# Kernel optimization log

Measured on AMD Instinct MI355X. Metric: run time of the kernel, lower is better.

The kernel has to match this reference:

```python
import jax, jax.numpy as jnp
import numpy as np

EPS = 1e-6

def _ln(x):
    # LayerNorm without affine, biased variance (matches torch default)
    m = jnp.mean(x, axis=-1, keepdims=True)
    v = jnp.var(x, axis=-1, keepdims=True)
    return (x - m) / jnp.sqrt(v + EPS)

def setup_inputs() -> dict:
    key = jax.random.key(0)
    ks = jax.random.split(key, 12)
    B, N, C = 8, 4096, 768
    H = C * 4
    s = 0.02
    return {
        "x":   jax.random.normal(ks[0], (B, N, C), dtype=jnp.float32),
        "Wq":  jax.random.normal(ks[1], (C, C), dtype=jnp.float32) * s,
        "bq":  jnp.zeros((C,), dtype=jnp.float32),
        "Wkv": jax.random.normal(ks[2], (C, 2 * C), dtype=jnp.float32) * s,
        "bkv": jnp.zeros((2 * C,), dtype=jnp.float32),
        "Wo":  jax.random.normal(ks[3], (C, C), dtype=jnp.float32) * s,
        "bo":  jnp.zeros((C,), dtype=jnp.float32),
        "W1":  jax.random.normal(ks[4], (C, H), dtype=jnp.float32) * s,
        "b1":  jnp.zeros((H,), dtype=jnp.float32),
        "W2":  jax.random.normal(ks[5], (H, C), dtype=jnp.float32) * s,
        "b2":  jnp.zeros((C,), dtype=jnp.float32),
    }

def reference(x, Wq, bq, Wkv, bkv, Wo, bo, W1, b1, W2, b2):
    B, N, C = x.shape
    h = 16
    d = C // h
    scale = d ** -0.5

    xn = _ln(x)                          # norm1 over full sequence
    past = xn[:, :-1, :]                 # [B, N-1, C]
    cur = xn[:, -1, :]                   # [B, C]

    q = (cur @ Wq + bq).reshape(B, h, 1, d)                 # [B,h,1,d]
    kv = past @ Wkv + bkv                                   # [B,N-1,2C]
    k, v = jnp.split(kv, 2, axis=-1)
    k = k.reshape(B, N - 1, h, d).transpose(0, 2, 1, 3)     # [B,h,N-1,d]
    v = v.reshape(B, N - 1, h, d).transpose(0, 2, 1, 3)

    sim = jnp.einsum('bhqd,bhkd->bhqk', q, k) * scale       # [B,h,1,N-1]
    attn = jax.nn.softmax(sim, axis=-1)
    out = jnp.einsum('bhqk,bhkd->bhqd', attn, v)            # [B,h,1,d]
    out = out.transpose(0, 2, 1, 3).reshape(B, C)           # [B,C]
    out = out @ Wo + bo

    last = x[:, -1, :] + out                                # attn residual
    mlp = jax.nn.gelu(_ln(last) @ W1 + b1, approximate=True) @ W2 + b2
    last = last + mlp                                       # mlp residual

    return x.at[:, -1, :].set(last)
```

## Files before the change

kernel.cpp:

```cpp
#include <hip/hip_runtime.h>

#define B_ 8
#define N_ 4096
#define C_ 768
#define NP_ 4095
#define H_ 16
#define D_ 48
#define HID_ 3072
#define SCALE 0.14433756729740643f

typedef unsigned short u16;
typedef unsigned int u32;
typedef __attribute__((ext_vector_type(4))) float f32x4;
typedef __attribute__((ext_vector_type(8))) short short8;

__device__ __forceinline__ u32 f2bf_bits(float f){
  union { float f; u32 i; } v; v.f = f;
  return (v.i + 0x7fffu + ((v.i >> 16) & 1u)) >> 16;
}
__device__ __forceinline__ u16 f2bf(float f){ return (u16)f2bf_bits(f); }
__device__ __forceinline__ u32 pack2(float a, float b){
  return f2bf_bits(a) | (f2bf_bits(b) << 16);
}

__global__ __launch_bounds__(256) void k_q(const float* __restrict__ x,
    const float* __restrict__ Wq, const float* __restrict__ bq,
    float* __restrict__ qv)
{
  int b = blockIdx.y, t = threadIdx.x;
  int j0 = blockIdx.x*32;
  __shared__ float xs[C_];
  __shared__ float red[32][9];
  __shared__ float redA[4], redB[4];
  const float* xr = x + ((size_t)b*N_ + NP_)*C_;
  float v0 = xr[t], v1 = xr[t+256], v2 = xr[t+512];
  float s = v0+v1+v2, q = v0*v0+v1*v1+v2*v2;
  #pragma unroll
  for (int off=32; off; off>>=1){ s += __shfl_xor(s,off); q += __shfl_xor(q,off); }
  int w = t>>6, l = t&63;
  if (l==0){ redA[w]=s; redB[w]=q; }
  __syncthreads();
  s = redA[0]+redA[1]+redA[2]+redA[3];
  q = redB[0]+redB[1]+redB[2]+redB[3];
  float mean = s*(1.f/C_), var = q*(1.f/C_) - mean*mean;
  float rstd = rsqrtf(var + 1e-6f);
  xs[t] = (v0-mean)*rstd; xs[t+256] = (v1-mean)*rstd; xs[t+512] = (v2-mean)*rstd;
  __syncthreads();
  int jl = t&31, part = t>>5;
  const float* wp = Wq + (size_t)(part*96)*C_ + j0 + jl;
  const float* xp = xs + part*96;
  float acc = 0.f;
  #pragma unroll 8
  for (int c=0;c<96;c++) acc += xp[c]*wp[(size_t)c*C_];
  red[jl][part] = acc;
  __syncthreads();
  if (part==0){
    float a = bq[j0+jl];
    #pragma unroll
    for (int p=0;p<8;p++) a += red[jl][p];
    qv[(size_t)b*C_ + j0 + jl] = a;
  }
}

__global__ __launch_bounds__(256) void k_qw(const float* __restrict__ qv,
    const float* __restrict__ Wkv, u16* __restrict__ qWb)
{
  int b = blockIdx.y, t = threadIdx.x;
  int c0 = blockIdx.x*16;
  __shared__ float qs[C_];
  for (int u=t; u<C_; u+=256) qs[u] = qv[(size_t)b*C_+u];
  __syncthreads();
  int h = t&15, cl = t>>4;
  int c = c0 + cl;
  const float* wp = Wkv + (size_t)c*(2*C_) + h*D_;
  const float* qh = qs + h*D_;
  float acc = 0.f;
  #pragma unroll
  for (int d=0; d<D_; d++) acc += qh[d]*wp[d];
  qWb[((size_t)b*H_ + h)*C_ + c] = f2bf(acc);
}

__global__ __launch_bounds__(256) void k_attn(const float* __restrict__ x,
    const u16* __restrict__ qWb, float* __restrict__ outp,
    float* __restrict__ ctx, float* __restrict__ denom)
{
  int b = blockIdx.y;
  int tid = threadIdx.x;
  int w = tid>>6, l = tid&63;
  int kblk = blockIdx.x*64;
  __shared__ float wexp[64][20];
  __shared__ float2 stl[64];
  const size_t xb = (size_t)b*N_*C_;

  #pragma unroll 4
  for (int it=0; it<16; ++it){
    int r = it*4 + w;
    int kt = kblk + r;
    const float4* rp = (const float4*)(x + xb + (size_t)kt*C_);
    float4* op = (float4*)(outp + xb + (size_t)kt*C_);
    float4 v0 = rp[l], v1 = rp[l+64], v2 = rp[l+128];
    op[l] = v0; op[l+64] = v1; op[l+128] = v2;
    float s = v0.x+v0.y+v0.z+v0.w + v1.x+v1.y+v1.z+v1.w + v2.x+v2.y+v2.z+v2.w;
    float q = v0.x*v0.x+v0.y*v0.y+v0.z*v0.z+v0.w*v0.w
            + v1.x*v1.x+v1.y*v1.y+v1.z*v1.z+v1.w*v1.w
            + v2.x*v2.x+v2.y*v2.y+v2.z*v2.z+v2.w*v2.w;
    #pragma unroll
    for (int off=32; off; off>>=1){ s += __shfl_xor(s,off); q += __shfl_xor(q,off); }
    if (l==0){
      float mean = s*(1.f/C_), var = q*(1.f/C_) - mean*mean;
      stl[r] = make_float2(mean, rsqrtf(var + 1e-6f));
    }
  }
  __syncthreads();

  {
    int arow = w*16 + (l&15);
    float2 ms = stl[arow];
    const float* ar = x + xb + (size_t)(kblk + arow)*C_ + (l>>4)*8;
    const u16* br = qWb + ((size_t)b*H_ + (l&15))*C_ + (l>>4)*8;
    f32x4 acc = {0.f,0.f,0.f,0.f};
    #pragma unroll 6
    for (int s2=0;s2<24;s2++){
      float4 g0 = *(const float4*)(ar + s2*32);
      float4 g1 = *(const float4*)(ar + s2*32 + 4);
      uint4 nv;
      nv.x = pack2((g0.x-ms.x)*ms.y, (g0.y-ms.x)*ms.y);
      nv.y = pack2((g0.z-ms.x)*ms.y, (g0.w-ms.x)*ms.y);
      nv.z = pack2((g1.x-ms.x)*ms.y, (g1.y-ms.x)*ms.y);
      nv.w = pack2((g1.z-ms.x)*ms.y, (g1.w-ms.x)*ms.y);
      union{uint4 u; short8 v;} A, Bf;
      A.u = nv;
      Bf.u = *(const uint4*)(br + s2*32);
      acc = __builtin_amdgcn_mfma_f32_16x16x32_bf16(A.v, Bf.v, acc, 0,0,0);
    }
    int hh = l&15, mb = (l>>4)*4;
    #pragma unroll
    for (int r=0;r<4;r++){
      int rr = w*16 + mb + r;
      int kt = kblk + rr;
      wexp[rr][hh] = (kt < NP_) ? __expf(acc[r]*SCALE) : 0.f;
    }
  }
  __syncthreads();

  if (tid < 16){
    float ds = 0.f;
    #pragma unroll 8
    for (int k=0;k<64;k++) ds += wexp[k][tid];
    atomicAdd(denom + (size_t)b*H_ + tid, ds);
  }

  int c0 = w*192;
  float accA[H_], accB[H_], accC[H_];
  #pragma unroll
  for (int h=0;h<H_;h++){ accA[h]=0.f; accB[h]=0.f; accC[h]=0.f; }
  for (int k=0;k<64;k++){
    int kt = kblk + k;
    const float* xr = x + xb + (size_t)kt*C_ + c0;
    float2 ms = stl[k];
    float xA = (xr[l]     - ms.x)*ms.y;
    float xB = (xr[l+64]  - ms.x)*ms.y;
    float xC = (xr[l+128] - ms.x)*ms.y;
    const float4* wp4 = (const float4*)&wexp[k][0];
    float4 w0 = wp4[0], w1 = wp4[1], w2 = wp4[2], w3 = wp4[3];
    accA[0]+=w0.x*xA; accA[1]+=w0.y*xA; accA[2]+=w0.z*xA; accA[3]+=w0.w*xA;
    accA[4]+=w1.x*xA; accA[5]+=w1.y*xA; accA[6]+=w1.z*xA; accA[7]+=w1.w*xA;
    accA[8]+=w2.x*xA; accA[9]+=w2.y*xA; accA[10]+=w2.z*xA; accA[11]+=w2.w*xA;
    accA[12]+=w3.x*xA; accA[13]+=w3.y*xA; accA[14]+=w3.z*xA; accA[15]+=w3.w*xA;
    accB[0]+=w0.x*xB; accB[1]+=w0.y*xB; accB[2]+=w0.z*xB; accB[3]+=w0.w*xB;
    accB[4]+=w1.x*xB; accB[5]+=w1.y*xB; accB[6]+=w1.z*xB; accB[7]+=w1.w*xB;
    accB[8]+=w2.x*xB; accB[9]+=w2.y*xB; accB[10]+=w2.z*xB; accB[11]+=w2.w*xB;
    accB[12]+=w3.x*xB; accB[13]+=w3.y*xB; accB[14]+=w3.z*xB; accB[15]+=w3.w*xB;
    accC[0]+=w0.x*xC; accC[1]+=w0.y*xC; accC[2]+=w0.z*xC; accC[3]+=w0.w*xC;
    accC[4]+=w1.x*xC; accC[5]+=w1.y*xC; accC[6]+=w1.z*xC; accC[7]+=w1.w*xC;
    accC[8]+=w2.x*xC; accC[9]+=w2.y*xC; accC[10]+=w2.z*xC; accC[11]+=w2.w*xC;
    accC[12]+=w3.x*xC; accC[13]+=w3.y*xC; accC[14]+=w3.z*xC; accC[15]+=w3.w*xC;
  }
  float* cb = ctx + (size_t)b*H_*C_;
  #pragma unroll
  for (int h=0;h<H_;h++){
    atomicAdd(cb + h*C_ + c0 + l,       accA[h]);
    atomicAdd(cb + h*C_ + c0 + 64 + l,  accB[h]);
    atomicAdd(cb + h*C_ + c0 + 128 + l, accC[h]);
  }
}

__global__ __launch_bounds__(256) void k_v(const float* __restrict__ ctx,
    const float* __restrict__ denom, const float* __restrict__ Wkv,
    const float* __restrict__ bkv, float* __restrict__ oat)
{
  int b = blockIdx.y, t = threadIdx.x;
  int t0 = blockIdx.x*32;
  int h0 = t0/D_;
  int h1 = (t0+31)/D_; if (h1 > H_-1) h1 = H_-1;
  __shared__ float cn[2][C_];
  __shared__ float red[32][9];
  float inv0 = 1.f/denom[(size_t)b*H_+h0];
  float inv1 = 1.f/denom[(size_t)b*H_+h1];
  for (int u=t; u<C_; u+=256){
    cn[0][u] = ctx[((size_t)b*H_+h0)*C_+u]*inv0;
    cn[1][u] = ctx[((size_t)b*H_+h1)*C_+u]*inv1;
  }
  __syncthreads();
  int jl = t&31, part = t>>5;
  int tt = t0 + jl;
  int hi = (tt/D_) - h0;
  const float* wp = Wkv + (size_t)(part*96)*(2*C_) + C_ + tt;
  const float* cp = cn[hi] + part*96;
  float acc = 0.f;
  #pragma unroll 8
  for (int c=0;c<96;c++) acc += cp[c]*wp[(size_t)c*(2*C_)];
  red[jl][part] = acc;
  __syncthreads();
  if (part==0){
    float a = bkv[C_ + tt];
    #pragma unroll
    for (int p=0;p<8;p++) a += red[jl][p];
    oat[(size_t)b*C_ + tt] = a;
  }
}

__global__ __launch_bounds__(256) void k_o(const float* __restrict__ x,
    const float* __restrict__ oat, const float* __restrict__ Wo,
    const float* __restrict__ bo, float* __restrict__ lastb)
{
  int b = blockIdx.y, t = threadIdx.x;
  int t0 = blockIdx.x*32;
  __shared__ float xs[C_];
  __shared__ float red[32][9];
  for (int u=t; u<C_; u+=256) xs[u] = oat[(size_t)b*C_+u];
  __syncthreads();
  int jl = t&31, part = t>>5;
  int tt = t0 + jl;
  const float* wp = Wo + (size_t)(part*96)*C_ + tt;
  const float* xp = xs + part*96;
  float acc = 0.f;
  #pragma unroll 8
  for (int c=0;c<96;c++) acc += xp[c]*wp[(size_t)c*C_];
  red[jl][part] = acc;
  __syncthreads();
  if (part==0){
    float a = bo[tt];
    #pragma unroll
    for (int p=0;p<8;p++) a += red[jl][p];
    lastb[(size_t)b*C_ + tt] = x[((size_t)b*N_ + NP_)*C_ + tt] + a;
  }
}

__global__ __launch_bounds__(256) void k_mlp1(const float* __restrict__ lastb,
    const float* __restrict__ W1, const float* __restrict__ b1,
    float* __restrict__ hid)
{
  int t = threadIdx.x;
  int j0 = blockIdx.x*16;
  __shared__ float xs[B_][C_];
  __shared__ float red[16][16][8];
  {
    int bb = t>>5, sub = t&31;
    const float* xr = lastb + (size_t)bb*C_;
    float s=0.f, q=0.f;
    #pragma unroll
    for (int j=0;j<24;j++){ float v = xr[sub+32*j]; s += v; q += v*v; }
    #pragma unroll
    for (int off=1; off<32; off<<=1){ s += __shfl_xor(s,off); q += __shfl_xor(q,off); }
    float mean = s*(1.f/C_), var = q*(1.f/C_) - mean*mean;
    float rstd = rsqrtf(var + 1e-6f);
    #pragma unroll
    for (int j=0;j<24;j++){ xs[bb][sub+32*j] = (xr[sub+32*j]-mean)*rstd; }
  }
  __syncthreads();
  int jl = t&15, part = t>>4;
  const float* wp = W1 + (size_t)(part*48)*HID_ + j0 + jl;
  float acc[B_];
  #pragma unroll
  for (int bb=0;bb<B_;bb++) acc[bb]=0.f;
  for (int c=0;c<48;c++){
    float wv = wp[(size_t)c*HID_];
    int cc = part*48 + c;
    #pragma unroll
    for (int bb=0;bb<B_;bb++) acc[bb] += xs[bb][cc]*wv;
  }
  #pragma unroll
  for (int bb=0;bb<B_;bb++) red[jl][part][bb] = acc[bb];
  __syncthreads();
  if (t < 128){
    int jl2 = t&15, bb = t>>4;
    float a = b1[j0+jl2];
    #pragma unroll
    for (int p=0;p<16;p++) a += red[jl2][p][bb];
    float t3 = a + 0.044715f*a*a*a;
    float g = 0.5f*a*(1.f + tanhf(0.7978845608f*t3));
    hid[(size_t)bb*HID_ + j0 + jl2] = g;
  }
}

__global__ __launch_bounds__(256) void k_mlp2(const float* __restrict__ hid,
    const float* __restrict__ W2, const float* __restrict__ b2,
    const float* __restrict__ lastb, float* __restrict__ outp)
{
  int t = threadIdx.x;
  int c0 = blockIdx.x*8;
  __shared__ float red[8][32][8];
  int ccl = t&7, part = t>>3;
  const float* wp = W2 + (size_t)(part*96)*C_ + c0 + ccl;
  float acc[B_];
  #pragma unroll
  for (int bb=0;bb<B_;bb++) acc[bb]=0.f;
  for (int j=0;j<96;j++){
    float wv = wp[(size_t)j*C_];
    int jj = part*96 + j;
    #pragma unroll
    for (int bb=0;bb<B_;bb++) acc[bb] += hid[(size_t)bb*HID_ + jj]*wv;
  }
  #pragma unroll
  for (int bb=0;bb<B_;bb++) red[ccl][part][bb] = acc[bb];
  __syncthreads();
  if (t < 64){
    int cc2 = t&7, bb = t>>3;
    float a = 0.f;
    #pragma unroll
    for (int p=0;p<32;p++) a += red[cc2][p][bb];
    int cc = c0 + cc2;
    a += b2[cc] + lastb[(size_t)bb*C_ + cc];
    outp[((size_t)bb*N_ + NP_)*C_ + cc] = a;
  }
}

extern "C" void kernel_launch(void* const* d_in, const int* in_sizes, int n_in,
                              void* d_out, int out_size, void* d_ws, size_t ws_size,
                              hipStream_t stream)
{
  (void)in_sizes; (void)n_in; (void)out_size; (void)ws_size;
  const float* x   = (const float*)d_in[0];
  const float* Wq  = (const float*)d_in[1];
  const float* bq  = (const float*)d_in[2];
  const float* Wkv = (const float*)d_in[3];
  const float* bkv = (const float*)d_in[4];
  const float* Wo  = (const float*)d_in[5];
  const float* bo  = (const float*)d_in[6];
  const float* W1  = (const float*)d_in[7];
  const float* b1  = (const float*)d_in[8];
  const float* W2  = (const float*)d_in[9];
  const float* b2  = (const float*)d_in[10];
  float* outp = (float*)d_out;
  float* ws = (float*)d_ws;
  float* ctx    = ws;
  float* denom  = ctx + 98304;
  float* qv     = denom + 128;
  float* oat    = qv + 6144;
  float* lastb  = oat + 6144;
  float* hid    = lastb + 6144;
  u16*   qWb    = (u16*)(hid + 24576);

  hipMemsetAsync(ctx, 0, (size_t)(98304+128)*sizeof(float), stream);
  hipLaunchKernelGGL(k_q,    dim3(24,B_), dim3(256), 0, stream, x, Wq, bq, qv);
  hipLaunchKernelGGL(k_qw,   dim3(48,B_), dim3(256), 0, stream, qv, Wkv, qWb);
  hipLaunchKernelGGL(k_attn, dim3(64,B_), dim3(256), 0, stream, x, qWb, outp, ctx, denom);
  hipLaunchKernelGGL(k_v,    dim3(24,B_), dim3(256), 0, stream, ctx, denom, Wkv, bkv, oat);
  hipLaunchKernelGGL(k_o,    dim3(24,B_), dim3(256), 0, stream, x, oat, Wo, bo, lastb);
  hipLaunchKernelGGL(k_mlp1, dim3(192), dim3(256), 0, stream, lastb, W1, b1, hid);
  hipLaunchKernelGGL(k_mlp2, dim3(96), dim3(256), 0, stream, hid, W2, b2, lastb, outp);
}
```

Measured before the change: 131.1 us.

## Split attention into score pass and MFMA context GEMM with mean correction

Replaces the single attention kernel with two passes. The first computes LayerNorm stats, writes normalized rows to LDS as bf16 for the score MFMA, and stores rstd-scaled softmax weights transposed in bf16 plus a per-head mean correction term. The second computes the context as an MFMA GEMM directly on raw x (converted to bf16), instead of per-thread scalar FMAs with 48 accumulators, and the mean term is subtracted later in k_v. This cuts ALU work and register pressure but adds a second read of x, a workspace round-trip, and bf16 rounding of raw x and the weights.

```diff
diff --git a/kernel.cpp b/kernel.cpp
--- a/kernel.cpp
+++ b/kernel.cpp
@@ -80,21 +80,22 @@
   qWb[((size_t)b*H_ + h)*C_ + c] = f2bf(acc);
 }
 
-__global__ __launch_bounds__(256) void k_attn(const float* __restrict__ x,
+__global__ __launch_bounds__(256) void k_pre(const float* __restrict__ x,
     const u16* __restrict__ qWb, float* __restrict__ outp,
-    float* __restrict__ ctx, float* __restrict__ denom)
+    u16* __restrict__ wrsT, float* __restrict__ denom, float* __restrict__ corr)
 {
   int b = blockIdx.y;
   int tid = threadIdx.x;
   int w = tid>>6, l = tid&63;
-  int kblk = blockIdx.x*64;
-  __shared__ float wexp[64][20];
-  __shared__ float2 stl[64];
+  int kblk = blockIdx.x*16;
+  __shared__ u16 xn[16][776];
+  __shared__ float2 stl[16];
+  __shared__ float part[4][16][17];
   const size_t xb = (size_t)b*N_*C_;
 
-  #pragma unroll 4
-  for (int it=0; it<16; ++it){
-    int r = it*4 + w;
+  #pragma unroll
+  for (int i=0;i<4;i++){
+    int r = w*4 + i;
     int kt = kblk + r;
     const float4* rp = (const float4*)(x + xb + (size_t)kt*C_);
     float4* op = (float4*)(outp + xb + (size_t)kt*C_);
@@ -106,88 +107,103 @@
             + v2.x*v2.x+v2.y*v2.y+v2.z*v2.z+v2.w*v2.w;
     #pragma unroll
     for (int off=32; off; off>>=1){ s += __shfl_xor(s,off); q += __shfl_xor(q,off); }
-    if (l==0){
-      float mean = s*(1.f/C_), var = q*(1.f/C_) - mean*mean;
-      stl[r] = make_float2(mean, rsqrtf(var + 1e-6f));
-    }
+    float mean = s*(1.f/C_), var = q*(1.f/C_) - mean*mean;
+    float rstd = rsqrtf(var + 1e-6f);
+    if (l==0) stl[r] = make_float2(mean, rstd);
+    u32* xrow = (u32*)&xn[r][0];
+    xrow[2*l]       = pack2((v0.x-mean)*rstd, (v0.y-mean)*rstd);
+    xrow[2*l+1]     = pack2((v0.z-mean)*rstd, (v0.w-mean)*rstd);
+    xrow[128+2*l]   = pack2((v1.x-mean)*rstd, (v1.y-mean)*rstd);
+    xrow[128+2*l+1] = pack2((v1.z-mean)*rstd, (v1.w-mean)*rstd);
+    xrow[256+2*l]   = pack2((v2.x-mean)*rstd, (v2.y-mean)*rstd);
+    xrow[256+2*l+1] = pack2((v2.z-mean)*rstd, (v2.w-mean)*rstd);
   }
   __syncthreads();
 
   {
-    int arow = w*16 + (l&15);
-    float2 ms = stl[arow];
-    const float* ar = x + xb + (size_t)(kblk + arow)*C_ + (l>>4)*8;
-    const u16* br = qWb + ((size_t)b*H_ + (l&15))*C_ + (l>>4)*8;
+    int arow = l&15;
+    int ko = w*192 + (l>>4)*8;
+    const u16* brb = qWb + ((size_t)b*H_ + (l&15))*C_ + ko;
     f32x4 acc = {0.f,0.f,0.f,0.f};
-    #pragma unroll 6
-    for (int s2=0;s2<24;s2++){
-      float4 g0 = *(const float4*)(ar + s2*32);
-      float4 g1 = *(const float4*)(ar + s2*32 + 4);
-      uint4 nv;
-      nv.x = pack2((g0.x-ms.x)*ms.y, (g0.y-ms.x)*ms.y);
-      nv.y = pack2((g0.z-ms.x)*ms.y, (g0.w-ms.x)*ms.y);
-      nv.z = pack2((g1.x-ms.x)*ms.y, (g1.y-ms.x)*ms.y);
-      nv.w = pack2((g1.z-ms.x)*ms.y, (g1.w-ms.x)*ms.y);
+    #pragma unroll
+    for (int s2=0;s2<6;s2++){
       union{uint4 u; short8 v;} A, Bf;
-      A.u = nv;
-      Bf.u = *(const uint4*)(br + s2*32);
+      A.u  = *(const uint4*)&xn[arow][ko + s2*32];
+      Bf.u = *(const uint4*)(brb + s2*32);
       acc = __builtin_amdgcn_mfma_f32_16x16x32_bf16(A.v, Bf.v, acc, 0,0,0);
     }
-    int hh = l&15, mb = (l>>4)*4;
-    #pragma unroll
-    for (int r=0;r<4;r++){
-      int rr = w*16 + mb + r;
-      int kt = kblk + rr;
-      wexp[rr][hh] = (kt < NP_) ? __expf(acc[r]*SCALE) : 0.f;
-    }
-  }
-  __syncthreads();
-
+    int mb = (l>>4)*4, n = l&15;
+    #pragma unroll
+    for (int r=0;r<4;r++) part[w][mb+r][n] = acc[r];
+  }
+  __syncthreads();
+
+  {
+    int m = tid>>4, n = tid&15;
+    float sim = part[0][m][n] + part[1][m][n] + part[2][m][n] + part[3][m][n];
+    int kt = kblk + m;
+    float2 ms = stl[m];
+    float wv = (kt < NP_) ? __expf(sim*SCALE) : 0.f;
+    float wrs = wv * ms.y;
+    wrsT[((size_t)b*H_ + n)*N_ + kt] = f2bf(wrs);
+    part[0][m][n] = wv;
+    part[1][m][n] = wrs * ms.x;
+  }
+  __syncthreads();
   if (tid < 16){
-    float ds = 0.f;
-    #pragma unroll 8
-    for (int k=0;k<64;k++) ds += wexp[k][tid];
+    float ds = 0.f, cs = 0.f;
+    #pragma unroll
+    for (int m=0;m<16;m++){ ds += part[0][m][tid]; cs += part[1][m][tid]; }
     atomicAdd(denom + (size_t)b*H_ + tid, ds);
-  }
-
-  int c0 = w*192;
-  float accA[H_], accB[H_], accC[H_];
-  #pragma unroll
-  for (int h=0;h<H_;h++){ accA[h]=0.f; accB[h]=0.f; accC[h]=0.f; }
-  for (int k=0;k<64;k++){
-    int kt = kblk + k;
-    const float* xr = x + xb + (size_t)kt*C_ + c0;
-    float2 ms = stl[k];
-    float xA = (xr[l]     - ms.x)*ms.y;
-    float xB = (xr[l+64]  - ms.x)*ms.y;
-    float xC = (xr[l+128] - ms.x)*ms.y;
-    const float4* wp4 = (const float4*)&wexp[k][0];
-    float4 w0 = wp4[0], w1 = wp4[1], w2 = wp4[2], w3 = wp4[3];
-    accA[0]+=w0.x*xA; accA[1]+=w0.y*xA; accA[2]+=w0.z*xA; accA[3]+=w0.w*xA;
-    accA[4]+=w1.x*xA; accA[5]+=w1.y*xA; accA[6]+=w1.z*xA; accA[7]+=w1.w*xA;
-    accA[8]+=w2.x*xA; accA[9]+=w2.y*xA; accA[10]+=w2.z*xA; accA[11]+=w2.w*xA;
-    accA[12]+=w3.x*xA; accA[13]+=w3.y*xA; accA[14]+=w3.z*xA; accA[15]+=w3.w*xA;
-    accB[0]+=w0.x*xB; accB[1]+=w0.y*xB; accB[2]+=w0.z*xB; accB[3]+=w0.w*xB;
-    accB[4]+=w1.x*xB; accB[5]+=w1.y*xB; accB[6]+=w1.z*xB; accB[7]+=w1.w*xB;
-    accB[8]+=w2.x*xB; accB[9]+=w2.y*xB; accB[10]+=w2.z*xB; accB[11]+=w2.w*xB;
-    accB[12]+=w3.x*xB; accB[13]+=w3.y*xB; accB[14]+=w3.z*xB; accB[15]+=w3.w*xB;
-    accC[0]+=w0.x*xC; accC[1]+=w0.y*xC; accC[2]+=w0.z*xC; accC[3]+=w0.w*xC;
-    accC[4]+=w1.x*xC; accC[5]+=w1.y*xC; accC[6]+=w1.z*xC; accC[7]+=w1.w*xC;
-    accC[8]+=w2.x*xC; accC[9]+=w2.y*xC; accC[10]+=w2.z*xC; accC[11]+=w2.w*xC;
-    accC[12]+=w3.x*xC; accC[13]+=w3.y*xC; accC[14]+=w3.z*xC; accC[15]+=w3.w*xC;
-  }
+    atomicAdd(corr  + (size_t)b*H_ + tid, cs);
+  }
+}
+
+__global__ __launch_bounds__(256) void k_ctx2(const float* __restrict__ x,
+    const u16* __restrict__ wrsT, float* __restrict__ ctx)
+{
+  int b = blockIdx.y;
+  int cg = blockIdx.x % 12;
+  int ks = blockIdx.x / 12;
+  int tid = threadIdx.x;
+  int w = tid>>6, l = tid&63;
+  int ctile = cg*64 + w*16;
+  int k0 = ks*512;
+  const size_t xb = (size_t)b*N_*C_;
+  const u16* ap = wrsT + ((size_t)b*H_ + (l&15))*N_ + k0 + (l>>4)*8;
+  const float* bp = x + xb + (size_t)(k0 + (l>>4)*8)*C_ + ctile + (l&15);
+  f32x4 acc = {0.f,0.f,0.f,0.f};
+  for (int s=0;s<16;s++){
+    union{uint4 u; short8 v;} A, Bf;
+    A.u = *(const uint4*)(ap + s*32);
+    const float* bq2 = bp + (size_t)s*32*C_;
+    float x0 = bq2[0];
+    float x1 = bq2[(size_t)1*C_];
+    float x2 = bq2[(size_t)2*C_];
+    float x3 = bq2[(size_t)3*C_];
+    float x4 = bq2[(size_t)4*C_];
+    float x5 = bq2[(size_t)5*C_];
+    float x6 = bq2[(size_t)6*C_];
+    float x7 = bq2[(size_t)7*C_];
+    uint4 nb;
+    nb.x = pack2(x0,x1); nb.y = pack2(x2,x3);
+    nb.z = pack2(x4,x5); nb.w = pack2(x6,x7);
+    Bf.u = nb;
+    acc = __builtin_amdgcn_mfma_f32_16x16x32_bf16(A.v, Bf.v, acc, 0,0,0);
+  }
+  int cc = ctile + (l&15);
   float* cb = ctx + (size_t)b*H_*C_;
   #pragma unroll
-  for (int h=0;h<H_;h++){
-    atomicAdd(cb + h*C_ + c0 + l,       accA[h]);
-    atomicAdd(cb + h*C_ + c0 + 64 + l,  accB[h]);
-    atomicAdd(cb + h*C_ + c0 + 128 + l, accC[h]);
+  for (int r=0;r<4;r++){
+    int h = (l>>4)*4 + r;
+    atomicAdd(cb + h*C_ + cc, acc[r]);
   }
 }
 
 __global__ __launch_bounds__(256) void k_v(const float* __restrict__ ctx,
-    const float* __restrict__ denom, const float* __restrict__ Wkv,
-    const float* __restrict__ bkv, float* __restrict__ oat)
+    const float* __restrict__ denom, const float* __restrict__ corr,
+    const float* __restrict__ Wkv, const float* __restrict__ bkv,
+    float* __restrict__ oat)
 {
   int b = blockIdx.y, t = threadIdx.x;
   int t0 = blockIdx.x*32;
@@ -197,9 +213,11 @@
   __shared__ float red[32][9];
   float inv0 = 1.f/denom[(size_t)b*H_+h0];
   float inv1 = 1.f/denom[(size_t)b*H_+h1];
+  float cr0 = corr[(size_t)b*H_+h0];
+  float cr1 = corr[(size_t)b*H_+h1];
   for (int u=t; u<C_; u+=256){
-    cn[0][u] = ctx[((size_t)b*H_+h0)*C_+u]*inv0;
-    cn[1][u] = ctx[((size_t)b*H_+h1)*C_+u]*inv1;
+    cn[0][u] = (ctx[((size_t)b*H_+h0)*C_+u] - cr0)*inv0;
+    cn[1][u] = (ctx[((size_t)b*H_+h1)*C_+u] - cr1)*inv1;
   }
   __syncthreads();
   int jl = t&31, part = t>>5;
@@ -346,17 +364,20 @@
   float* ws = (float*)d_ws;
   float* ctx    = ws;
   float* denom  = ctx + 98304;
-  float* qv     = denom + 128;
+  float* corr   = denom + 128;
+  float* qv     = corr + 128;
   float* oat    = qv + 6144;
   float* lastb  = oat + 6144;
   float* hid    = lastb + 6144;
   u16*   qWb    = (u16*)(hid + 24576);
-
-  hipMemsetAsync(ctx, 0, (size_t)(98304+128)*sizeof(float), stream);
+  u16*   wrsT   = (u16*)(hid + 24576 + 49152);
+
+  hipMemsetAsync(ctx, 0, (size_t)(98304+256)*sizeof(float), stream);
   hipLaunchKernelGGL(k_q,    dim3(24,B_), dim3(256), 0, stream, x, Wq, bq, qv);
   hipLaunchKernelGGL(k_qw,   dim3(48,B_), dim3(256), 0, stream, qv, Wkv, qWb);
-  hipLaunchKernelGGL(k_attn, dim3(64,B_), dim3(256), 0, stream, x, qWb, outp, ctx, denom);
-  hipLaunchKernelGGL(k_v,    dim3(24,B_), dim3(256), 0, stream, ctx, denom, Wkv, bkv, oat);
+  hipLaunchKernelGGL(k_pre,  dim3(256,B_), dim3(256), 0, stream, x, qWb, outp, wrsT, denom, corr);
+  hipLaunchKernelGGL(k_ctx2, dim3(96,B_), dim3(256), 0, stream, x, wrsT, ctx);
+  hipLaunchKernelGGL(k_v,    dim3(24,B_), dim3(256), 0, stream, ctx, denom, corr, Wkv, bkv, oat);
   hipLaunchKernelGGL(k_o,    dim3(24,B_), dim3(256), 0, stream, x, oat, Wo, bo, lastb);
   hipLaunchKernelGGL(k_mlp1, dim3(192), dim3(256), 0, stream, lastb, W1, b1, hid);
   hipLaunchKernelGGL(k_mlp2, dim3(96), dim3(256), 0, stream, hid, W2, b2, lastb, outp);
```

Result: faster. 110.0 us (-16.1%).
